# Kernel tuning notes

Measured on AMD Instinct MI355X. Metric: run time of the kernel, lower is better.

The kernel has to match this reference:

```python
import jax, jax.numpy as jnp
import numpy as np

FACTOR = 5

def setup_inputs() -> dict:
    key = jax.random.key(0)
    kq, kk, kv, ki = jax.random.split(key, 4)
    B, L, H, D = 8, 2048, 8, 64
    u = FACTOR * int(np.ceil(np.log(L)))  # sample_k == n_top == 40
    return {
        "queries": jax.random.normal(kq, (B, L, H, D), dtype=jnp.float32),
        "keys": jax.random.normal(kk, (B, L, H, D), dtype=jnp.float32),
        "values": jax.random.normal(kv, (B, L, H, D), dtype=jnp.float32),
        "index_sample": jax.random.randint(ki, (L, u), 0, L, dtype=jnp.int32),
    }

def reference(queries, keys, values, index_sample):
    B, L, H, D = queries.shape
    # faithful to torch .view(B, H, -1, D) on contiguous tensors (a reshape, not a transpose)
    q = queries.reshape(B, H, L, D)
    k = keys.reshape(B, H, L, D)
    v = values.reshape(B, H, L, D)
    u = FACTOR * int(np.ceil(np.log(L)))  # U_part == u
    # --- _prob_QK: sample keys per query, score, pick top-u queries ---
    K_sample = k[:, :, index_sample, :]                      # [B,H,L,u,D] gather over L_K
    QK_sample = jnp.einsum('bhld,bhlsd->bhls', q, K_sample)  # [B,H,L,u]
    M = QK_sample.max(axis=-1) - QK_sample.sum(axis=-1) / L  # sparsity measure [B,H,L]
    M_top = jax.lax.top_k(M, u)[1]                           # [B,H,u] indices of active queries
    Q_reduce = jnp.take_along_axis(q, M_top[..., None], axis=2)  # [B,H,u,D]
    scores = jnp.einsum('bhud,bhld->bhul', Q_reduce, k)      # [B,H,u,L]
    scale = 1.0 / float(np.sqrt(D))
    attn = jax.nn.softmax(scores * scale, axis=-1)           # dropout is identity in eval
    context = jnp.einsum('bhul,bhld->bhud', attn, v)         # [B,H,u,D]
    return context, attn
```

## Files before the change

### kernel.cpp

```cpp
#include <hip/hip_runtime.h>
#include <math.h>

#define LSEQ 2048
#define DDIM 64
#define UU   40
#define NBH  64
#define NCHUNK 16
#define CROWS  128
#define CTX_ELEMS (NBH*UU*DDIM)

__device__ __forceinline__ float grp8_sum(float x) {
  float t;
  t = __int_as_float(__builtin_amdgcn_update_dpp(0, __float_as_int(x), 0xB1, 0xF, 0xF, false));
  x += t;
  t = __int_as_float(__builtin_amdgcn_update_dpp(0, __float_as_int(x), 0x4E, 0xF, 0xF, false));
  x += t;
  t = __int_as_float(__builtin_amdgcn_update_dpp(0, __float_as_int(x), 0x141, 0xF, 0xF, false));
  x += t;
  return x;
}

__global__ __launch_bounds__(256) void k0_sort(
    const int* __restrict__ idxs, int* __restrict__ sidx, int* __restrict__ soff) {
  int l = blockIdx.x * 4 + (threadIdx.x >> 6);
  int lane = threadIdx.x & 63;
  int v = 0, c = NCHUNK;
  if (lane < UU) { v = idxs[l * UU + lane]; c = v >> 7; }
  unsigned long long lower = (1ull << lane) - 1ull;
  int base = 0;
#pragma unroll
  for (int cc = 0; cc < NCHUNK; ++cc) {
    unsigned long long m = __ballot(c == cc);
    if (c == cc) {
      int rank = __popcll(m & lower);
      sidx[l * UU + base + rank] = v;
    }
    int cnt = __popcll(m);
    if (lane == cc) soff[l * NCHUNK + cc] = (base << 8) | cnt;
    base += cnt;
  }
}

__global__ __launch_bounds__(512, 8) void k12_gather(
    const float* __restrict__ q, const float* __restrict__ k,
    const int* __restrict__ sidx, const int* __restrict__ soff,
    float2* __restrict__ Mpart) {
  __shared__ float4 kt[CROWS * 16];
  int b = blockIdx.x;
  int bh = b & 63;
  int c  = b >> 6;
  int t  = threadIdx.x;

  {
    const float4* src = (const float4*)(k + ((size_t)bh * LSEQ + c * CROWS) * DDIM);
#pragma unroll
    for (int j = 0; j < 4; ++j) kt[t + 512 * j] = src[t + 512 * j];
  }
  __syncthreads();

  int w = t >> 6;
  int lane = t & 63;
  int g = lane >> 3;
  int sub = lane & 7;

#pragma unroll 1
  for (int lb = 0; lb < 256; lb += 8) {
    int l = w * 256 + lb + g;
    const float4* qr = (const float4*)(q + ((size_t)bh * LSEQ + l) * DDIM);
    float4 qa = qr[sub];
    float4 qb = qr[sub + 8];
    int oc   = soff[l * NCHUNK + c];
    int cnt  = oc & 255;
    int base = oc >> 8;
    const int* sp = sidx + l * UU + base;
    int rowv[8];
#pragma unroll
    for (int s = 0; s < 8; ++s) rowv[s] = sp[s] & (CROWS - 1);
    float mx = -INFINITY, sm = 0.f;
#pragma unroll
    for (int s = 0; s < 8; ++s) {
      if (s == 0 || __any(s < cnt)) {
        if (s < cnt) {
          const float4* kr = kt + rowv[s] * 16;
          float4 a  = kr[sub];
          float4 bq = kr[sub + 8];
          float d = qa.x * a.x + qa.y * a.y + qa.z * a.z + qa.w * a.w
                  + qb.x * bq.x + qb.y * bq.y + qb.z * bq.z + qb.w * bq.w;
          d = grp8_sum(d);
          mx = fmaxf(mx, d);
          sm += d;
        }
      }
    }
    for (int s = 8; s < cnt; ++s) {
      int row = sp[s] & (CROWS - 1);
      const float4* kr = kt + row * 16;
      float4 a  = kr[sub];
      float4 bq = kr[sub + 8];
      float d = qa.x * a.x + qa.y * a.y + qa.z * a.z + qa.w * a.w
              + qb.x * bq.x + qb.y * bq.y + qb.z * bq.z + qb.w * bq.w;
      d = grp8_sum(d);
      mx = fmaxf(mx, d);
      sm += d;
    }
    if (sub == 0) Mpart[((size_t)bh * NCHUNK + c) * LSEQ + l] = make_float2(mx, sm);
  }
}

__global__ __launch_bounds__(256) void k3_topk(const float2* __restrict__ Mp,
                                               int* __restrict__ Mtop) {
  int bh = blockIdx.x;
  int t = threadIdx.x;
  int w = t >> 6;
  int lane = t & 63;
  float v[8];
#pragma unroll
  for (int j = 0; j < 8; ++j) {
    int l = t + 256 * j;
    float mxv = -INFINITY, smv = 0.f;
#pragma unroll
    for (int c = 0; c < NCHUNK; ++c) {
      float2 p = Mp[((size_t)bh * NCHUNK + c) * LSEQ + l];
      mxv = fmaxf(mxv, p.x);
      smv += p.y;
    }
    v[j] = mxv - smv * (1.0f / (float)LSEQ);
  }
  __shared__ float swv[4];
  __shared__ int   swi[4];
  __shared__ int   win;
  for (int it = 0; it < UU; ++it) {
    float bv = -INFINITY; int bi = 0x7fffffff;
#pragma unroll
    for (int j = 0; j < 8; ++j) {
      if (v[j] > bv) { bv = v[j]; bi = t + 256 * j; }
    }
#pragma unroll
    for (int off = 32; off > 0; off >>= 1) {
      float ov = __shfl_xor(bv, off, 64);
      int   oi = __shfl_xor(bi, off, 64);
      if (ov > bv || (ov == bv && oi < bi)) { bv = ov; bi = oi; }
    }
    if (lane == 0) { swv[w] = bv; swi[w] = bi; }
    __syncthreads();
    if (t == 0) {
      float fv = swv[0]; int fi = swi[0];
#pragma unroll
      for (int j = 1; j < 4; ++j) {
        if (swv[j] > fv || (swv[j] == fv && swi[j] < fi)) { fv = swv[j]; fi = swi[j]; }
      }
      Mtop[bh * UU + it] = fi;
      win = fi;
    }
    __syncthreads();
    int wi = win;
#pragma unroll
    for (int j = 0; j < 8; ++j)
      if (wi == t + 256 * j) v[j] = -INFINITY;
  }
}

__global__ __launch_bounds__(256, 3) void k457_fused(
    const float* __restrict__ q, const float* __restrict__ k,
    const float* __restrict__ v, const int* __restrict__ Mtop,
    float* __restrict__ attn, float* __restrict__ ctx) {
  __shared__ float  sct[4 * LSEQ];
  __shared__ float4 vt4[64 * 16];
  int b = blockIdx.x;
  int bh = b & 63;
  int u0 = (b >> 6) * 4;
  int t = threadIdx.x;

  {
    int g = t >> 2;
    int sub = t & 3;
    float4 qv[4][4];
#pragma unroll
    for (int u = 0; u < 4; ++u) {
      int qi = Mtop[bh * UU + u0 + u];
      const float4* qr = (const float4*)(q + (size_t)(bh * LSEQ + qi) * DDIM);
#pragma unroll
      for (int m = 0; m < 4; ++m) qv[u][m] = qr[4 * m + sub];
    }
    const float* kb = k + (size_t)bh * LSEQ * DDIM;
#pragma unroll 1
    for (int p = 0; p < 32; ++p) {
      int l = p * 64 + g;
      const float4* kr = (const float4*)(kb + (size_t)l * DDIM);
      float4 ks[4];
#pragma unroll
      for (int m = 0; m < 4; ++m) ks[m] = kr[4 * m + sub];
      float d[4];
#pragma unroll
      for (int u = 0; u < 4; ++u) {
        float s = 0.f;
#pragma unroll
        for (int m = 0; m < 4; ++m) {
          float4 x = qv[u][m], a = ks[m];
          s += x.x * a.x + x.y * a.y + x.z * a.z + x.w * a.w;
        }
        s += __shfl_xor(s, 1, 64);
        s += __shfl_xor(s, 2, 64);
        d[u] = s * 0.125f;
      }
      if (sub == 0) {
#pragma unroll
        for (int u = 0; u < 4; ++u) sct[u * LSEQ + l] = d[u];
      }
    }
  }
  __syncthreads();

  int w = t >> 6, lane = t & 63;
  {
    float* row = sct + w * LSEQ;
    float vv[32];
    float mx = -INFINITY;
#pragma unroll
    for (int j = 0; j < 32; ++j) { vv[j] = row[lane + 64 * j]; mx = fmaxf(mx, vv[j]); }
#pragma unroll
    for (int off = 32; off > 0; off >>= 1) mx = fmaxf(mx, __shfl_xor(mx, off, 64));
    float sm = 0.f;
#pragma unroll
    for (int j = 0; j < 32; ++j) { vv[j] = __expf(vv[j] - mx); sm += vv[j]; }
#pragma unroll
    for (int off = 32; off > 0; off >>= 1) sm += __shfl_xor(sm, off, 64);
    float inv = 1.0f / sm;
    float* ap = attn + (size_t)(bh * UU + u0 + w) * LSEQ;
#pragma unroll
    for (int j = 0; j < 32; ++j) {
      float a = vv[j] * inv;
      row[lane + 64 * j] = a;
      ap[lane + 64 * j] = a;
    }
  }
  __syncthreads();

  int dq = lane & 15;
  int lq = lane >> 4;
  float4 acc[4];
#pragma unroll
  for (int u = 0; u < 4; ++u) acc[u] = make_float4(0.f, 0.f, 0.f, 0.f);

  const float4* vsrc = (const float4*)(v + (size_t)bh * LSEQ * DDIM);
#pragma unroll 1
  for (int tile = 0; tile < 32; ++tile) {
#pragma unroll
    for (int i = 0; i < 4; ++i) {
      int idx = t + 256 * i;
      int row = idx >> 4, c4 = idx & 15;
      vt4[row * 16 + (c4 ^ (row & 3))] = vsrc[tile * 1024 + idx];
    }
    __syncthreads();
#pragma unroll
    for (int i = 0; i < 4; ++i) {
      int r = w * 16 + i * 4 + lq;
      int l = tile * 64 + r;
      float4 vv4 = vt4[r * 16 + (dq ^ (r & 3))];
#pragma unroll
      for (int u = 0; u < 4; ++u) {
        float a = sct[u * LSEQ + l];
        acc[u].x += a * vv4.x;
        acc[u].y += a * vv4.y;
        acc[u].z += a * vv4.z;
        acc[u].w += a * vv4.w;
      }
    }
    __syncthreads();
  }

#pragma unroll
  for (int u = 0; u < 4; ++u) {
    acc[u].x += __shfl_xor(acc[u].x, 16, 64);
    acc[u].y += __shfl_xor(acc[u].y, 16, 64);
    acc[u].z += __shfl_xor(acc[u].z, 16, 64);
    acc[u].w += __shfl_xor(acc[u].w, 16, 64);
    acc[u].x += __shfl_xor(acc[u].x, 32, 64);
    acc[u].y += __shfl_xor(acc[u].y, 32, 64);
    acc[u].z += __shfl_xor(acc[u].z, 32, 64);
    acc[u].w += __shfl_xor(acc[u].w, 32, 64);
  }
  __syncthreads();
  float* pacc = (float*)vt4;
  if (lq == 0) {
#pragma unroll
    for (int u = 0; u < 4; ++u)
      ((float4*)pacc)[(w * 4 + u) * 16 + dq] = acc[u];
  }
  __syncthreads();
  {
    int uu = t >> 6, d = t & 63;
    float s = pacc[(0 * 4 + uu) * 64 + d] + pacc[(1 * 4 + uu) * 64 + d]
            + pacc[(2 * 4 + uu) * 64 + d] + pacc[(3 * 4 + uu) * 64 + d];
    ctx[((size_t)bh * UU + u0 + uu) * DDIM + d] = s;
  }
}

extern "C" void kernel_launch(void* const* d_in, const int* in_sizes, int n_in,
                              void* d_out, int out_size, void* d_ws, size_t ws_size,
                              hipStream_t stream) {
  const float* q   = (const float*)d_in[0];
  const float* k   = (const float*)d_in[1];
  const float* v   = (const float*)d_in[2];
  const int*   idx = (const int*)d_in[3];

  float* ctx  = (float*)d_out;
  float* attn = (float*)d_out + CTX_ELEMS;
  float2* Mpart = (float2*)attn;

  int* sidx = (int*)d_ws;
  int* soff = sidx + LSEQ * UU + 16;
  int* Mtop = soff + LSEQ * NCHUNK;

  k0_sort<<<LSEQ / 4, 256, 0, stream>>>(idx, sidx, soff);
  k12_gather<<<NBH * NCHUNK, 512, 0, stream>>>(q, k, sidx, soff, Mpart);
  k3_topk<<<NBH, 256, 0, stream>>>(Mpart, Mtop);
  k457_fused<<<NBH * 10, 256, 0, stream>>>(q, k, v, Mtop, attn, ctx);
}
```

Baseline: 293.1 us.

## Reorder queries per chunk by sample count to reduce wave divergence in gather

Adds a small kernel that, for each key chunk, bucket-sorts query rows by how many sampled keys fall into that chunk (descending), writing a per-chunk permutation. The gather kernel then walks queries in that order, so the 8 queries sharing a wavefront have similar counts and the __any-guarded loop wastes fewer iterations. Queries with zero samples in the chunk also skip loading q rows and sample indices. The cost is an extra launch, an indirect order lookup and less contiguous q loads.

New measurement: 304.5 us. 1.04x slower.

```diff
diff --git a/kernel.cpp b/kernel.cpp
--- a/kernel.cpp
+++ b/kernel.cpp
@@ -41,10 +41,38 @@
   }
 }
 
+__global__ __launch_bounds__(256) void k0_order(
+    const int* __restrict__ soff, int* __restrict__ order) {
+  int c = blockIdx.x;
+  int t = threadIdx.x;
+  __shared__ int hist[48];
+  __shared__ int pos[48];
+  if (t < 48) hist[t] = 0;
+  __syncthreads();
+  int cl[8];
+#pragma unroll
+  for (int j = 0; j < 8; ++j) {
+    int l = t + 256 * j;
+    cl[j] = soff[l * NCHUNK + c] & 255;
+    atomicAdd(&hist[cl[j]], 1);
+  }
+  __syncthreads();
+  if (t == 0) {
+    int run = 0;
+    for (int x = 40; x >= 0; --x) { pos[x] = run; run += hist[x]; }
+  }
+  __syncthreads();
+#pragma unroll
+  for (int j = 0; j < 8; ++j) {
+    int p = atomicAdd(&pos[cl[j]], 1);
+    order[c * LSEQ + p] = t + 256 * j;
+  }
+}
+
 __global__ __launch_bounds__(512, 8) void k12_gather(
     const float* __restrict__ q, const float* __restrict__ k,
     const int* __restrict__ sidx, const int* __restrict__ soff,
-    float2* __restrict__ Mpart) {
+    const int* __restrict__ order, float2* __restrict__ Mpart) {
   __shared__ float4 kt[CROWS * 16];
   int b = blockIdx.x;
   int bh = b & 63;
@@ -65,21 +93,24 @@
 
 #pragma unroll 1
   for (int lb = 0; lb < 256; lb += 8) {
-    int l = w * 256 + lb + g;
-    const float4* qr = (const float4*)(q + ((size_t)bh * LSEQ + l) * DDIM);
-    float4 qa = qr[sub];
-    float4 qb = qr[sub + 8];
+    int l = order[c * LSEQ + w * 256 + lb + g];
     int oc   = soff[l * NCHUNK + c];
     int cnt  = oc & 255;
     int base = oc >> 8;
-    const int* sp = sidx + l * UU + base;
-    int rowv[8];
-#pragma unroll
-    for (int s = 0; s < 8; ++s) rowv[s] = sp[s] & (CROWS - 1);
+    float4 qa = make_float4(0.f, 0.f, 0.f, 0.f), qb = qa;
+    int rowv[8] = {0, 0, 0, 0, 0, 0, 0, 0};
+    if (cnt > 0) {
+      const float4* qr = (const float4*)(q + ((size_t)bh * LSEQ + l) * DDIM);
+      qa = qr[sub];
+      qb = qr[sub + 8];
+      const int* sp = sidx + l * UU + base;
+#pragma unroll
+      for (int s = 0; s < 8; ++s) rowv[s] = sp[s] & (CROWS - 1);
+    }
     float mx = -INFINITY, sm = 0.f;
 #pragma unroll
     for (int s = 0; s < 8; ++s) {
-      if (s == 0 || __any(s < cnt)) {
+      if (__any(s < cnt)) {
         if (s < cnt) {
           const float4* kr = kt + rowv[s] * 16;
           float4 a  = kr[sub];
@@ -93,7 +124,7 @@
       }
     }
     for (int s = 8; s < cnt; ++s) {
-      int row = sp[s] & (CROWS - 1);
+      int row = sidx[l * UU + base + s] & (CROWS - 1);
       const float4* kr = kt + row * 16;
       float4 a  = kr[sub];
       float4 bq = kr[sub + 8];
@@ -308,12 +339,14 @@
   float* attn = (float*)d_out + CTX_ELEMS;
   float2* Mpart = (float2*)attn;
 
-  int* sidx = (int*)d_ws;
-  int* soff = sidx + LSEQ * UU + 16;
-  int* Mtop = soff + LSEQ * NCHUNK;
+  int* sidx  = (int*)d_ws;
+  int* soff  = sidx + LSEQ * UU + 16;
+  int* Mtop  = soff + LSEQ * NCHUNK;
+  int* order = Mtop + NBH * UU;
 
   k0_sort<<<LSEQ / 4, 256, 0, stream>>>(idx, sidx, soff);
-  k12_gather<<<NBH * NCHUNK, 512, 0, stream>>>(q, k, sidx, soff, Mpart);
+  k0_order<<<NCHUNK, 256, 0, stream>>>(soff, order);
+  k12_gather<<<NBH * NCHUNK, 512, 0, stream>>>(q, k, sidx, soff, order, Mpart);
   k3_topk<<<NBH, 256, 0, stream>>>(Mpart, Mtop);
   k457_fused<<<NBH * 10, 256, 0, stream>>>(q, k, v, Mtop, attn, ctx);
 }
```

## Process eight selected queries per block in fused attention and split gather launch

Applied to the files above, without the earlier changes.

The fused scores/softmax/context kernel now handles 8 selected queries per block instead of 4. This halves the grid to 320 blocks and halves how often K and V are re-read per head, at the cost of more shared memory and registers and an occupancy hint lowered to 2. The QK dot product switches to an 8-lane DPP group reduction. The gather kernel is split into two launches of 512 blocks each with a block offset, plus minor changes to how sample indices are loaded.

New measurement: 341.2 us. 1.16x slower.

```diff
diff --git a/kernel.cpp b/kernel.cpp
--- a/kernel.cpp
+++ b/kernel.cpp
@@ -44,9 +44,9 @@
 __global__ __launch_bounds__(512, 8) void k12_gather(
     const float* __restrict__ q, const float* __restrict__ k,
     const int* __restrict__ sidx, const int* __restrict__ soff,
-    float2* __restrict__ Mpart) {
+    float2* __restrict__ Mpart, int boff) {
   __shared__ float4 kt[CROWS * 16];
-  int b = blockIdx.x;
+  int b = blockIdx.x + boff;
   int bh = b & 63;
   int c  = b >> 6;
   int t  = threadIdx.x;
@@ -79,7 +79,7 @@
     float mx = -INFINITY, sm = 0.f;
 #pragma unroll
     for (int s = 0; s < 8; ++s) {
-      if (s == 0 || __any(s < cnt)) {
+      if (__any(s < cnt)) {
         if (s < cnt) {
           const float4* kr = kt + rowv[s] * 16;
           float4 a  = kr[sub];
@@ -93,7 +93,7 @@
       }
     }
     for (int s = 8; s < cnt; ++s) {
-      int row = sp[s] & (CROWS - 1);
+      int row = sidx[l * UU + base + s] & (CROWS - 1);
       const float4* kr = kt + row * 16;
       float4 a  = kr[sub];
       float4 bq = kr[sub + 8];
@@ -160,60 +160,50 @@
   }
 }
 
-__global__ __launch_bounds__(256, 3) void k457_fused(
+__global__ __launch_bounds__(256, 2) void k457_fused(
     const float* __restrict__ q, const float* __restrict__ k,
     const float* __restrict__ v, const int* __restrict__ Mtop,
     float* __restrict__ attn, float* __restrict__ ctx) {
-  __shared__ float  sct[4 * LSEQ];
+  __shared__ float  sct[8 * LSEQ];
   __shared__ float4 vt4[64 * 16];
   int b = blockIdx.x;
   int bh = b & 63;
-  int u0 = (b >> 6) * 4;
+  int u0 = (b >> 6) * 8;
   int t = threadIdx.x;
+  int w = t >> 6, lane = t & 63;
 
   {
-    int g = t >> 2;
-    int sub = t & 3;
-    float4 qv[4][4];
-#pragma unroll
-    for (int u = 0; u < 4; ++u) {
+    int g = t >> 3;
+    int sub = t & 7;
+    float4 qa[8], qb[8];
+#pragma unroll
+    for (int u = 0; u < 8; ++u) {
       int qi = Mtop[bh * UU + u0 + u];
       const float4* qr = (const float4*)(q + (size_t)(bh * LSEQ + qi) * DDIM);
-#pragma unroll
-      for (int m = 0; m < 4; ++m) qv[u][m] = qr[4 * m + sub];
+      qa[u] = qr[sub];
+      qb[u] = qr[sub + 8];
     }
     const float* kb = k + (size_t)bh * LSEQ * DDIM;
 #pragma unroll 1
-    for (int p = 0; p < 32; ++p) {
-      int l = p * 64 + g;
+    for (int p = 0; p < 64; ++p) {
+      int l = p * 32 + g;
       const float4* kr = (const float4*)(kb + (size_t)l * DDIM);
-      float4 ks[4];
-#pragma unroll
-      for (int m = 0; m < 4; ++m) ks[m] = kr[4 * m + sub];
-      float d[4];
-#pragma unroll
-      for (int u = 0; u < 4; ++u) {
-        float s = 0.f;
-#pragma unroll
-        for (int m = 0; m < 4; ++m) {
-          float4 x = qv[u][m], a = ks[m];
-          s += x.x * a.x + x.y * a.y + x.z * a.z + x.w * a.w;
-        }
-        s += __shfl_xor(s, 1, 64);
-        s += __shfl_xor(s, 2, 64);
-        d[u] = s * 0.125f;
+      float4 ka = kr[sub];
+      float4 kc = kr[sub + 8];
+#pragma unroll
+      for (int u = 0; u < 8; ++u) {
+        float s = qa[u].x * ka.x + qa[u].y * ka.y + qa[u].z * ka.z + qa[u].w * ka.w
+                + qb[u].x * kc.x + qb[u].y * kc.y + qb[u].z * kc.z + qb[u].w * kc.w;
+        s = grp8_sum(s);
+        if (sub == 0) sct[u * LSEQ + l] = s * 0.125f;
       }
-      if (sub == 0) {
-#pragma unroll
-        for (int u = 0; u < 4; ++u) sct[u * LSEQ + l] = d[u];
-      }
-    }
-  }
-  __syncthreads();
-
-  int w = t >> 6, lane = t & 63;
-  {
-    float* row = sct + w * LSEQ;
+    }
+  }
+  __syncthreads();
+
+#pragma unroll 1
+  for (int uu = w * 2; uu < w * 2 + 2; ++uu) {
+    float* row = sct + uu * LSEQ;
     float vv[32];
     float mx = -INFINITY;
 #pragma unroll
@@ -226,7 +216,7 @@
 #pragma unroll
     for (int off = 32; off > 0; off >>= 1) sm += __shfl_xor(sm, off, 64);
     float inv = 1.0f / sm;
-    float* ap = attn + (size_t)(bh * UU + u0 + w) * LSEQ;
+    float* ap = attn + (size_t)(bh * UU + u0 + uu) * LSEQ;
 #pragma unroll
     for (int j = 0; j < 32; ++j) {
       float a = vv[j] * inv;
@@ -238,9 +228,9 @@
 
   int dq = lane & 15;
   int lq = lane >> 4;
-  float4 acc[4];
-#pragma unroll
-  for (int u = 0; u < 4; ++u) acc[u] = make_float4(0.f, 0.f, 0.f, 0.f);
+  float4 acc[8];
+#pragma unroll
+  for (int u = 0; u < 8; ++u) acc[u] = make_float4(0.f, 0.f, 0.f, 0.f);
 
   const float4* vsrc = (const float4*)(v + (size_t)bh * LSEQ * DDIM);
 #pragma unroll 1
@@ -258,7 +248,7 @@
       int l = tile * 64 + r;
       float4 vv4 = vt4[r * 16 + (dq ^ (r & 3))];
 #pragma unroll
-      for (int u = 0; u < 4; ++u) {
+      for (int u = 0; u < 8; ++u) {
         float a = sct[u * LSEQ + l];
         acc[u].x += a * vv4.x;
         acc[u].y += a * vv4.y;
@@ -270,7 +260,7 @@
   }
 
 #pragma unroll
-  for (int u = 0; u < 4; ++u) {
+  for (int u = 0; u < 8; ++u) {
     acc[u].x += __shfl_xor(acc[u].x, 16, 64);
     acc[u].y += __shfl_xor(acc[u].y, 16, 64);
     acc[u].z += __shfl_xor(acc[u].z, 16, 64);
@@ -284,14 +274,16 @@
   float* pacc = (float*)vt4;
   if (lq == 0) {
 #pragma unroll
-    for (int u = 0; u < 4; ++u)
-      ((float4*)pacc)[(w * 4 + u) * 16 + dq] = acc[u];
-  }
-  __syncthreads();
-  {
-    int uu = t >> 6, d = t & 63;
-    float s = pacc[(0 * 4 + uu) * 64 + d] + pacc[(1 * 4 + uu) * 64 + d]
-            + pacc[(2 * 4 + uu) * 64 + d] + pacc[(3 * 4 + uu) * 64 + d];
+    for (int u = 0; u < 8; ++u)
+      ((float4*)pacc)[(w * 8 + u) * 16 + dq] = acc[u];
+  }
+  __syncthreads();
+#pragma unroll
+  for (int j = 0; j < 2; ++j) {
+    int idx = t + 256 * j;
+    int uu = idx >> 6, d = idx & 63;
+    float s = pacc[(0 * 8 + uu) * 64 + d] + pacc[(1 * 8 + uu) * 64 + d]
+            + pacc[(2 * 8 + uu) * 64 + d] + pacc[(3 * 8 + uu) * 64 + d];
     ctx[((size_t)bh * UU + u0 + uu) * DDIM + d] = s;
   }
 }
@@ -308,12 +300,13 @@
   float* attn = (float*)d_out + CTX_ELEMS;
   float2* Mpart = (float2*)attn;
 
-  int* sidx = (int*)d_ws;
-  int* soff = sidx + LSEQ * UU + 16;
-  int* Mtop = soff + LSEQ * NCHUNK;
+  int* sidx  = (int*)d_ws;
+  int* soff  = sidx + LSEQ * UU + 16;
+  int* Mtop  = soff + LSEQ * NCHUNK;
 
   k0_sort<<<LSEQ / 4, 256, 0, stream>>>(idx, sidx, soff);
-  k12_gather<<<NBH * NCHUNK, 512, 0, stream>>>(q, k, sidx, soff, Mpart);
+  k12_gather<<<512, 512, 0, stream>>>(q, k, sidx, soff, Mpart, 0);
+  k12_gather<<<512, 512, 0, stream>>>(q, k, sidx, soff, Mpart, 512);
   k3_topk<<<NBH, 256, 0, stream>>>(Mpart, Mtop);
-  k457_fused<<<NBH * 10, 256, 0, stream>>>(q, k, v, Mtop, attn, ctx);
-}
+  k457_fused<<<NBH * 5, 256, 0, stream>>>(q, k, v, Mtop, attn, ctx);
+}
```
